# Kernel optimization log

Measured on AMD Instinct MI355X. Metric: run time of the kernel, lower is better.

Reference implementation:

```python
import jax, jax.numpy as jnp
import numpy as np

NEG_INF = -1e9


def setup_inputs() -> dict:
    key = jax.random.key(0)
    k1, k2, k3, k4 = jax.random.split(key, 4)
    B, S, U, D = 512, 200, 50, 32
    current_user_embedding = jax.random.normal(k1, (B, D), dtype=jnp.float32)
    similar_user_embedding = jax.random.normal(k2, (B, S, U, D), dtype=jnp.float32)
    current_item_embedding = jax.random.normal(k3, (B, S, D), dtype=jnp.float32)
    mask = jax.random.randint(k4, (B, S, U), 0, 2) == 1  # True = masked out
    return {
        "current_user_embedding": current_user_embedding,
        "similar_user_embedding": similar_user_embedding,
        "current_item_embedding": current_item_embedding,
        "mask": mask,
    }


def reference(current_user_embedding, similar_user_embedding, current_item_embedding, mask):
    # scores: [B, S, U] -- dot product of current user with each similar user
    # (avoids the explicit repeat to [B,S,U,D] in the torch code)
    scores = jnp.einsum("bd,bsud->bsu", current_user_embedding, similar_user_embedding)
    scores = jnp.where(mask, NEG_INF, scores)
    attn = jax.nn.softmax(scores, axis=2)  # over similar_user_len
    # weighted sum of similar-user values: [B, S, D]
    out = jnp.einsum("bsu,bsud->bsd", attn, similar_user_embedding)
    return out + current_item_embedding
```

## Files before the change

### kernel.cpp

```cpp
#include <hip/hip_runtime.h>
#include <math.h>


#define NEG_INF_F (-1e9f)

constexpr int B = 512, S = 200, U = 50, D = 32;
constexpr int TILES = B * S;
constexpr int TILE_F4 = U * D / 4;
constexpr int SUE_F4 = TILES * TILE_F4;

__global__ __launch_bounds__(256) void DIB_69861938037647_kernel(
    const float* __restrict__ cu,
    const float* __restrict__ sue,
    const float* __restrict__ cie,
    const int*   __restrict__ mask,
    float* __restrict__ out)
{
    const int lane = threadIdx.x & 63;
    const int wave = threadIdx.x >> 6;
    const int tile = blockIdx.x * 4 + wave;

    const int g  = lane >> 3;
    const int d0 = (lane & 7) * 4;

    const float4* sue4 = (const float4*)sue;
    float4 v[7];
    const int base4 = tile * TILE_F4;
    #pragma unroll
    for (int j = 0; j < 7; ++j) {
        int gi = base4 + j * 64 + lane;
        gi = min(gi, SUE_F4 - 1);
        v[j] = sue4[gi];
    }

    const int b = tile / S;
    const float4 c4 = *(const float4*)(cu + b * D + d0);

    float sc[7];
    #pragma unroll
    for (int j = 0; j < 7; ++j) {
        float p = v[j].x * c4.x + v[j].y * c4.y + v[j].z * c4.z + v[j].w * c4.w;
        p += __shfl_xor(p, 1);
        p += __shfl_xor(p, 2);
        p += __shfl_xor(p, 4);
        sc[j] = p;
    }

    const int mrow = tile * U;
    #pragma unroll
    for (int j = 0; j < 7; ++j) {
        const int u = j * 8 + g;
        if (u < U) {
            if (mask[mrow + u]) sc[j] = NEG_INF_F;
        } else {
            sc[j] = -INFINITY;
        }
    }

    float m = sc[0];
    #pragma unroll
    for (int j = 1; j < 7; ++j) m = fmaxf(m, sc[j]);
    m = fmaxf(m, __shfl_xor(m, 8));
    m = fmaxf(m, __shfl_xor(m, 16));
    m = fmaxf(m, __shfl_xor(m, 32));

    float e[7];
    float tsum = 0.f;
    #pragma unroll
    for (int j = 0; j < 7; ++j) {
        e[j] = __expf(sc[j] - m);
        tsum += e[j];
    }
    tsum += __shfl_xor(tsum, 8);
    tsum += __shfl_xor(tsum, 16);
    tsum += __shfl_xor(tsum, 32);
    const float inv = 1.0f / tsum;

    float4 o = make_float4(0.f, 0.f, 0.f, 0.f);
    #pragma unroll
    for (int j = 0; j < 7; ++j) {
        const float a = e[j] * inv;
        o.x += a * v[j].x; o.y += a * v[j].y; o.z += a * v[j].z; o.w += a * v[j].w;
    }
    #pragma unroll
    for (int msk = 8; msk <= 32; msk <<= 1) {
        o.x += __shfl_xor(o.x, msk);
        o.y += __shfl_xor(o.y, msk);
        o.z += __shfl_xor(o.z, msk);
        o.w += __shfl_xor(o.w, msk);
    }

    if (g == 0) {
        const float4 ci = *(const float4*)(cie + tile * D + d0);
        float4 r = make_float4(o.x + ci.x, o.y + ci.y, o.z + ci.z, o.w + ci.w);
        *(float4*)(out + tile * D + d0) = r;
    }
}

extern "C" void kernel_launch(void* const* d_in, const int* in_sizes, int n_in,
                              void* d_out, int out_size, void* d_ws, size_t ws_size,
                              hipStream_t stream) {
    const float* cu   = (const float*)d_in[0];
    const float* sue  = (const float*)d_in[1];
    const float* cie  = (const float*)d_in[2];
    const int*   mask = (const int*)d_in[3];
    float* out = (float*)d_out;

    DIB_69861938037647_kernel<<<TILES / 4, 256, 0, stream>>>(cu, sue, cie, mask, out);
}
```

Measured before the change: 843.9 us.

## Use persistent waves with double-buffered register prefetch of tiles

```diff
diff --git a/kernel.cpp b/kernel.cpp
--- a/kernel.cpp
+++ b/kernel.cpp
@@ -9,52 +9,55 @@
 constexpr int TILE_F4 = U * D / 4;
 constexpr int SUE_F4 = TILES * TILE_F4;
 
-__global__ __launch_bounds__(256) void DIB_69861938037647_kernel(
-    const float* __restrict__ cu,
-    const float* __restrict__ sue,
-    const float* __restrict__ cie,
-    const int*   __restrict__ mask,
-    float* __restrict__ out)
+constexpr int BLOCKS = 1600;
+constexpr int NWAVES = BLOCKS * 4;
+
+struct TileBuf {
+    float4 v[7];
+    int    mk[7];
+    float4 c4;
+    float4 ci;
+};
+
+__device__ __forceinline__ void prefetch_tile(
+    int tile, int lane, int g, int d0,
+    const float4* __restrict__ sue4, const float* __restrict__ cu,
+    const float* __restrict__ cie, const int* __restrict__ mask,
+    TileBuf& tb)
 {
-    const int lane = threadIdx.x & 63;
-    const int wave = threadIdx.x >> 6;
-    const int tile = blockIdx.x * 4 + wave;
-
-    const int g  = lane >> 3;
-    const int d0 = (lane & 7) * 4;
-
-    const float4* sue4 = (const float4*)sue;
-    float4 v[7];
     const int base4 = tile * TILE_F4;
     #pragma unroll
     for (int j = 0; j < 7; ++j) {
         int gi = base4 + j * 64 + lane;
         gi = min(gi, SUE_F4 - 1);
-        v[j] = sue4[gi];
+        tb.v[j] = sue4[gi];
     }
-
-    const int b = tile / S;
-    const float4 c4 = *(const float4*)(cu + b * D + d0);
-
-    float sc[7];
-    #pragma unroll
-    for (int j = 0; j < 7; ++j) {
-        float p = v[j].x * c4.x + v[j].y * c4.y + v[j].z * c4.z + v[j].w * c4.w;
-        p += __shfl_xor(p, 1);
-        p += __shfl_xor(p, 2);
-        p += __shfl_xor(p, 4);
-        sc[j] = p;
-    }
-
     const int mrow = tile * U;
     #pragma unroll
     for (int j = 0; j < 7; ++j) {
         const int u = j * 8 + g;
-        if (u < U) {
-            if (mask[mrow + u]) sc[j] = NEG_INF_F;
-        } else {
-            sc[j] = -INFINITY;
-        }
+        tb.mk[j] = (u < U) ? mask[mrow + u] : 1;
+    }
+    const int b = tile / S;
+    tb.c4 = *(const float4*)(cu + b * D + d0);
+    tb.ci = *(const float4*)(cie + tile * D + d0);
+}
+
+__device__ __forceinline__ void compute_tile(
+    int tile, int g, int d0, const TileBuf& tb, float* __restrict__ out)
+{
+    float sc[7];
+    #pragma unroll
+    for (int j = 0; j < 7; ++j) {
+        float p = tb.v[j].x * tb.c4.x + tb.v[j].y * tb.c4.y
+                + tb.v[j].z * tb.c4.z + tb.v[j].w * tb.c4.w;
+        p += __shfl_xor(p, 1);
+        p += __shfl_xor(p, 2);
+        p += __shfl_xor(p, 4);
+        const int u = j * 8 + g;
+        if (u >= U)        p = -INFINITY;
+        else if (tb.mk[j]) p = NEG_INF_F;
+        sc[j] = p;
     }
 
     float m = sc[0];
@@ -80,7 +83,8 @@
     #pragma unroll
     for (int j = 0; j < 7; ++j) {
         const float a = e[j] * inv;
-        o.x += a * v[j].x; o.y += a * v[j].y; o.z += a * v[j].z; o.w += a * v[j].w;
+        o.x += a * tb.v[j].x; o.y += a * tb.v[j].y;
+        o.z += a * tb.v[j].z; o.w += a * tb.v[j].w;
     }
     #pragma unroll
     for (int msk = 8; msk <= 32; msk <<= 1) {
@@ -91,9 +95,41 @@
     }
 
     if (g == 0) {
-        const float4 ci = *(const float4*)(cie + tile * D + d0);
-        float4 r = make_float4(o.x + ci.x, o.y + ci.y, o.z + ci.z, o.w + ci.w);
+        float4 r = make_float4(o.x + tb.ci.x, o.y + tb.ci.y,
+                               o.z + tb.ci.z, o.w + tb.ci.w);
         *(float4*)(out + tile * D + d0) = r;
+    }
+}
+
+__global__ __launch_bounds__(256) void DIB_69861938037647_kernel(
+    const float* __restrict__ cu,
+    const float* __restrict__ sue,
+    const float* __restrict__ cie,
+    const int*   __restrict__ mask,
+    float* __restrict__ out)
+{
+    const int lane = threadIdx.x & 63;
+    const int wid  = (blockIdx.x << 2) + (threadIdx.x >> 6);
+    const int g    = lane >> 3;
+    const int d0   = (lane & 7) * 4;
+
+    const float4* sue4 = (const float4*)sue;
+
+    TileBuf bufA, bufB;
+    int t = wid;
+    prefetch_tile(t, lane, g, d0, sue4, cu, cie, mask, bufA);
+
+    #pragma unroll 1
+    for (int it = 0; it < 8; ++it) {
+        const int t1 = t + NWAVES;
+        prefetch_tile(t1, lane, g, d0, sue4, cu, cie, mask, bufB);
+        compute_tile(t, g, d0, bufA, out);
+
+        const int t2 = t1 + NWAVES;
+        if (t2 < TILES)
+            prefetch_tile(t2, lane, g, d0, sue4, cu, cie, mask, bufA);
+        compute_tile(t1, g, d0, bufB, out);
+        t = t2;
     }
 }
 
@@ -106,5 +142,5 @@
     const int*   mask = (const int*)d_in[3];
     float* out = (float*)d_out;
 
-    DIB_69861938037647_kernel<<<TILES / 4, 256, 0, stream>>>(cu, sue, cie, mask, out);
+    DIB_69861938037647_kernel<<<BLOCKS, 256, 0, stream>>>(cu, sue, cie, mask, out);
 }
```

Result: no change. 858.7 us (+1.8%).
